# Kernel optimization log

Hardware: AMD Instinct MI355X
Metric: run time of the kernel (lower is better)

The kernel has to match this reference:

```python
import jax, jax.numpy as jnp
import numpy as np

STRIDES = (8, 16, 32)
NC = 80            # num_classes
BINS = 16          # dfl_bins
TOPK = 10          # tal_topk
TAL_ALPHA, TAL_BETA = 0.5, 6.0   # ultralytics TaskAlignedAssigner defaults
EPS = 1e-9
FOCAL_A, FOCAL_G = 0.25, 2.0
W_CLS, W_IOU, W_DFL = 0.5, 7.5, 1.5


def _make_grid(H, W, stride):
    ys, xs = jnp.meshgrid(jnp.arange(H, dtype=jnp.float32), jnp.arange(W, dtype=jnp.float32), indexing='ij')
    return jnp.stack([(xs + 0.5) * stride, (ys + 0.5) * stride], -1).reshape(H * W, 2)


def _flatten(p):
    # (B,C,H,W) -> cls (B,N,NC), dfl (B,N,4,BINS); channel layout = [4*BINS dfl | NC cls]
    B, C, H, W = p.shape
    p = p.transpose(0, 2, 3, 1).reshape(B, H * W, C)
    return p[..., 4 * BINS:], p[..., :4 * BINS].reshape(B, H * W, 4, BINS)


def _pairwise_iou(gt, pr):
    # gt (B,G,4), pr (B,N,4) -> iou (B,G,N)
    g = gt[:, :, None]
    p = pr[:, None]
    lt = jnp.maximum(g[..., :2], p[..., :2])
    rb = jnp.minimum(g[..., 2:], p[..., 2:])
    wh = jnp.clip(rb - lt, 0.0)
    inter = wh[..., 0] * wh[..., 1]
    ag = (g[..., 2] - g[..., 0]) * (g[..., 3] - g[..., 1])
    ap = jnp.clip(p[..., 2] - p[..., 0], 0.0) * jnp.clip(p[..., 3] - p[..., 1], 0.0)
    return inter / (ag + ap - inter + EPS)


def _ciou_loss(p, t):
    # elementwise CIoU loss, (...,4) xyxy -> (...)
    px1, py1, px2, py2 = p[..., 0], p[..., 1], p[..., 2], p[..., 3]
    tx1, ty1, tx2, ty2 = t[..., 0], t[..., 1], t[..., 2], t[..., 3]
    w1, h1 = px2 - px1, py2 - py1
    w2, h2 = tx2 - tx1, ty2 - ty1
    inter = jnp.clip(jnp.minimum(px2, tx2) - jnp.maximum(px1, tx1), 0.0) * \
            jnp.clip(jnp.minimum(py2, ty2) - jnp.maximum(py1, ty1), 0.0)
    union = w1 * h1 + w2 * h2 - inter + EPS
    iou = inter / union
    cw = jnp.maximum(px2, tx2) - jnp.minimum(px1, tx1)
    ch = jnp.maximum(py2, ty2) - jnp.minimum(py1, ty1)
    c2 = cw * cw + ch * ch + EPS
    rho2 = ((px1 + px2 - tx1 - tx2) ** 2 + (py1 + py2 - ty1 - ty2) ** 2) / 4.0
    v = (4.0 / np.pi ** 2) * (jnp.arctan(w2 / (h2 + EPS)) - jnp.arctan(w1 / (h1 + EPS))) ** 2
    alpha = jax.lax.stop_gradient(v / (v - iou + (1.0 + EPS)))
    return 1.0 - (iou - rho2 / c2 - v * alpha)


def _tal_assign(cls_prob, pred_boxes, grids, gt_bboxes, gt_labels):
    B, N, C = cls_prob.shape
    G = gt_bboxes.shape[1]
    idx = jnp.broadcast_to(gt_labels[:, None, :], (B, N, G))
    scores = jnp.take_along_axis(cls_prob, idx, axis=2).transpose(0, 2, 1)  # (B,G,N)
    overlaps = _pairwise_iou(gt_bboxes, pred_boxes)                          # (B,G,N)
    align = scores ** TAL_ALPHA * overlaps ** TAL_BETA
    x, y = grids[:, 0], grids[:, 1]
    in_gts = ((x[None, None] > gt_bboxes[..., 0:1]) & (x[None, None] < gt_bboxes[..., 2:3]) &
              (y[None, None] > gt_bboxes[..., 1:2]) & (y[None, None] < gt_bboxes[..., 3:4]))
    metric = jnp.where(in_gts, align, 0.0)
    vals, idxs = jax.lax.top_k(metric, TOPK)                                 # (B,G,TOPK)
    bi = jnp.arange(B)[:, None, None]
    gi = jnp.arange(G)[None, :, None]
    topk_mask = jnp.zeros((B, G, N), bool).at[bi, gi, idxs].set(vals > EPS)
    mask_pos = topk_mask & in_gts
    multi = mask_pos.sum(1) > 1                                              # (B,N)
    is_max = jnp.argmax(overlaps, 1)[:, None, :] == jnp.arange(G)[None, :, None]
    mask_pos = jnp.where(multi[:, None, :], is_max, mask_pos)
    fg = mask_pos.any(1)                                                     # (B,N)
    matched = jnp.argmax(mask_pos, 1)                                        # (B,N)
    mi = jnp.where(fg, matched, -1)
    b2 = jnp.arange(B)[:, None]
    tb = gt_bboxes[b2, matched]                                              # (B,N,4)
    tl = gt_labels[b2, matched]                                              # (B,N)
    mpf = mask_pos.astype(align.dtype)
    align_m = align * mpf
    ov_m = overlaps * mpf
    norm = (align_m * ov_m.max(-1, keepdims=True) / (align_m.max(-1, keepdims=True) + EPS)).max(1)
    ts = jax.nn.one_hot(tl, C, dtype=align.dtype) * norm[..., None] * fg[..., None]
    return ts, tb, fg, mi


def _dfl_targets(gt_bboxes, mi, fgf, grids, stride_map):
    # vectorized version of _make_dfl_targets: soft two-bin scatter per coord
    B, N = mi.shape
    b2 = jnp.arange(B)[:, None]
    boxes = gt_bboxes[b2, jnp.maximum(mi, 0)]                                # (B,N,4)
    cx, cy = grids[:, 0], grids[:, 1]
    d = jnp.stack([jnp.clip(cx - boxes[..., 0], 0.0), jnp.clip(cy - boxes[..., 1], 0.0),
                   jnp.clip(boxes[..., 2] - cx, 0.0), jnp.clip(boxes[..., 3] - cy, 0.0)], -1)
    d = jnp.clip(d / stride_map[None, :, None], 0.0, BINS - 1 - 1e-6)
    lo = jnp.floor(d)
    a = d - lo
    lo_i = lo.astype(jnp.int32)
    up_i = jnp.minimum(lo_i + 1, BINS - 1)
    td = jax.nn.one_hot(lo_i, BINS) * (1.0 - a)[..., None] + jax.nn.one_hot(up_i, BINS) * a[..., None]
    return td * fgf[..., None, None]                                         # (B,N,4,BINS)


def _focal_sum(logits, targets):
    logits = logits.reshape(-1, NC)
    targets = targets.reshape(-1, NC)
    p = jax.nn.sigmoid(logits)
    # stable BCE-with-logits
    ce = jnp.maximum(logits, 0.0) - logits * targets + jnp.log1p(jnp.exp(-jnp.abs(logits)))
    p_t = p * targets + (1.0 - p) * (1.0 - targets)
    a_t = targets * FOCAL_A + (1.0 - targets) * (1.0 - FOCAL_A)
    return (a_t * (1.0 - p_t) ** FOCAL_G * ce).sum()


def _loss(p0, p1, p2, gt_bboxes, gt_labels):
    cls_l, dfl_l, grid_l, str_l = [], [], [], []
    for p, s in zip((p0, p1, p2), STRIDES):
        c, d = _flatten(p)
        cls_l.append(c)
        dfl_l.append(d)
        H, W = p.shape[2], p.shape[3]
        grid_l.append(_make_grid(H, W, s))
        str_l.append(jnp.full((H * W,), float(s), jnp.float32))
    all_cls = jnp.concatenate(cls_l, 1)       # (B,N,NC)
    all_dfl = jnp.concatenate(dfl_l, 1)       # (B,N,4,BINS)
    grids = jnp.concatenate(grid_l, 0)        # (N,2)
    stride_map = jnp.concatenate(str_l, 0)    # (N,)
    # DFL decode: expectation over bins * stride -> ltrb -> xyxy
    dist = (jax.nn.softmax(all_dfl, -1) * jnp.arange(BINS, dtype=jnp.float32)).sum(-1) * stride_map[None, :, None]
    cx, cy = grids[:, 0], grids[:, 1]
    pred_boxes = jnp.stack([cx - dist[..., 0], cy - dist[..., 1], cx + dist[..., 2], cy + dist[..., 3]], -1)
    # assignment under stop_gradient (torch.no_grad in the original)
    cls_prob = jax.lax.stop_gradient(jax.nn.sigmoid(all_cls))
    pb_sg = jax.lax.stop_gradient(pred_boxes)
    ts, tb, fg, mi = _tal_assign(cls_prob, pb_sg, grids, gt_bboxes, gt_labels)
    ts = jax.lax.stop_gradient(ts)
    tb = jax.lax.stop_gradient(tb)
    fgf = fg.astype(jnp.float32)
    den = jnp.maximum(fg.sum(), 1).astype(jnp.float32)
    loss_iou = (_ciou_loss(pred_boxes, tb) * fgf).sum() / den
    tdfl = _dfl_targets(gt_bboxes, mi, fgf, grids, stride_map)
    loss_dfl = -(tdfl * jax.nn.log_softmax(all_dfl, -1)).sum() / den
    loss_cls = _focal_sum(all_cls, ts) / den
    return jnp.stack([W_IOU * loss_iou, W_DFL * loss_dfl, W_CLS * loss_cls])


def setup_inputs() -> dict:
    key = jax.random.key(0)
    ks = jax.random.split(key, 5)
    B, G = 16, 32
    p0 = jax.random.normal(ks[0], (B, 4 * BINS + NC, 80, 80), jnp.float32)
    p1 = jax.random.normal(ks[1], (B, 4 * BINS + NC, 40, 40), jnp.float32)
    p2 = jax.random.normal(ks[2], (B, 4 * BINS + NC, 20, 20), jnp.float32)
    u = jax.random.uniform(ks[3], (B, G, 4), jnp.float32)
    x1 = u[..., 0] * 560.0
    y1 = u[..., 1] * 560.0
    w = u[..., 2] * 140.0 + 20.0
    h = u[..., 3] * 140.0 + 20.0
    gt_bboxes = jnp.stack([x1, y1, jnp.minimum(x1 + w, 640.0), jnp.minimum(y1 + h, 640.0)], -1)
    gt_labels = jax.random.randint(ks[4], (B, G), 0, NC, jnp.int32)
    return {"p0": p0, "p1": p1, "p2": p2, "gt_bboxes": gt_bboxes, "gt_labels": gt_labels}


def reference(p0, p1, p2, gt_bboxes, gt_labels):
    return _loss(p0, p1, p2, gt_bboxes, gt_labels)
```

## Files before the change

kernel.cpp:

```cpp
#include <hip/hip_runtime.h>
#include <hip/hip_bf16.h>
#include <math.h>

#define NCC 80
#define BINS 16
#define NCH 144
#define NB 16
#define NG 32
#define NA 8400
#define HW0 6400
#define HW1 1600
#define HW2 400
#define TOPKK 10
#define EPSF 1e-9f
#define MAXC 832
#define MAXFG (NB*NG*TOPKK)
#define FGB (MAXFG/4)
#define NMASK (NB*NA)
#define DEC_BLOCKS 525
#define FOCAL_BLOCKS 2625
#define MAIN_BLOCKS (DEC_BLOCKS + FOCAL_BLOCKS)

__device__ __forceinline__ void anchor_geom(int n, float& cx, float& cy, float& st){
    if(n < HW0){ int y=n/80, x=n-y*80; st=8.f; cx=(x+0.5f)*8.f; cy=(y+0.5f)*8.f; }
    else if(n < HW0+HW1){ int m=n-HW0; int y=m/40, x=m-y*40; st=16.f; cx=(x+0.5f)*16.f; cy=(y+0.5f)*16.f; }
    else { int m=n-(HW0+HW1); int y=m/20, x=m-y*20; st=32.f; cx=(x+0.5f)*32.f; cy=(y+0.5f)*32.f; }
}

__device__ __forceinline__ const float* level_base(const float* p0, const float* p1, const float* p2,
                                                   int b, int n, int& m, int& hw){
    if(n < HW0){ m=n; hw=HW0; return p0 + (size_t)b*NCH*HW0; }
    if(n < HW0+HW1){ m=n-HW0; hw=HW1; return p1 + (size_t)b*NCH*HW1; }
    m=n-(HW0+HW1); hw=HW2; return p2 + (size_t)b*NCH*HW2;
}

__device__ __forceinline__ float iou_gp(float gx1,float gy1,float gx2,float gy2,
                                        float px1,float py1,float px2,float py2){
    float ltx = fmaxf(gx1, px1), lty = fmaxf(gy1, py1);
    float rbx = fminf(gx2, px2), rby = fminf(gy2, py2);
    float w = fmaxf(rbx-ltx, 0.f), h = fmaxf(rby-lty, 0.f);
    float inter = w*h;
    float ag = (gx2-gx1)*(gy2-gy1);
    float ap = fmaxf(px2-px1,0.f)*fmaxf(py2-py1,0.f);
    return inter/(ag+ap-inter+EPSF);
}

__device__ __forceinline__ float focal0(float x, float& p, float& ce0){
    float ax = fabsf(x);
    float e  = __expf(-ax);
    float r  = 1.f/(1.f+e);
    p   = (x >= 0.f) ? r : 1.f - r;
    ce0 = fmaxf(x,0.f) + __logf(1.f+e);
    return 0.75f*p*p*ce0;
}

__global__ __launch_bounds__(256) void k_main(const float* __restrict__ p0, const float* __restrict__ p1,
                                              const float* __restrict__ p2, float* __restrict__ boxc,
                                              unsigned* __restrict__ maskg, float* __restrict__ amax,
                                              float* __restrict__ omax, int* __restrict__ cnt,
                                              int* __restrict__ done, float* __restrict__ pcls){
    int tid = threadIdx.x;
    if(blockIdx.x < DEC_BLOCKS){
        int l = blockIdx.x*256 + tid;
        maskg[l] = 0u;
        if(l < NB*NG){ amax[l] = 0.f; omax[l] = 0.f; }
        if(l == 0){ *cnt = 0; *done = 0; }
        int q = l % 2100;
        int j = (l / 2100) & 3;
        int b = l / 8400;
        const float* pl; int hw, m, n0, D; float st;
        if(q < 1600){ pl=p0; hw=HW0; m=4*q;        n0=m;         D=80; st=8.f; }
        else if(q < 2000){ pl=p1; hw=HW1; m=4*(q-1600); n0=HW0+m;     D=40; st=16.f; }
        else { pl=p2; hw=HW2; m=4*(q-2000); n0=HW0+HW1+m; D=20; st=32.f; }
        const float* ch = pl + ((size_t)b*NCH + j*BINS)*hw + m;
        float4 v[BINS];
        float4 mx = make_float4(-1e30f,-1e30f,-1e30f,-1e30f);
        #pragma unroll
        for(int k=0;k<BINS;k++){
            v[k] = *(const float4*)(ch + (size_t)k*hw);
            mx.x=fmaxf(mx.x,v[k].x); mx.y=fmaxf(mx.y,v[k].y);
            mx.z=fmaxf(mx.z,v[k].z); mx.w=fmaxf(mx.w,v[k].w);
        }
        float4 s = make_float4(0,0,0,0), acc = make_float4(0,0,0,0);
        #pragma unroll
        for(int k=0;k<BINS;k++){
            float fk=(float)k; float e;
            e=__expf(v[k].x-mx.x); s.x+=e; acc.x+=e*fk;
            e=__expf(v[k].y-mx.y); s.y+=e; acc.y+=e*fk;
            e=__expf(v[k].z-mx.z); s.z+=e; acc.z+=e*fk;
            e=__expf(v[k].w-mx.w); s.w+=e; acc.w+=e*fk;
        }
        float4 d = make_float4(acc.x/s.x*st, acc.y/s.y*st, acc.z/s.z*st, acc.w/s.w*st);
        int row = m / D, col = m - row*D;
        float cy = (row+0.5f)*st;
        float cx0=(col+0.5f)*st, cx1=(col+1.5f)*st, cx2=(col+2.5f)*st, cx3=(col+3.5f)*st;
        float4 o;
        if(j==0)      o = make_float4(cx0-d.x, cx1-d.y, cx2-d.z, cx3-d.w);
        else if(j==1) o = make_float4(cy -d.x, cy -d.y, cy -d.z, cy -d.w);
        else if(j==2) o = make_float4(cx0+d.x, cx1+d.y, cx2+d.z, cx3+d.w);
        else          o = make_float4(cy +d.x, cy +d.y, cy +d.z, cy +d.w);
        *(float4*)(boxc + (size_t)j*NB*NA + (size_t)b*NA + n0) = o;
    } else {
        __shared__ float s4[4];
        int blk = blockIdx.x - DEC_BLOCKS;
        int t = blk*256 + tid;
        float acc = 0.f;
        #pragma unroll
        for(int it=0; it<4; ++it){
            int i4 = t + it*672000;
            const float4* src;
            if(i4 < 2048000){
                int b = i4 / 128000; int r = i4 - b*128000;
                src = (const float4*)(p0 + (size_t)b*921600 + 409600) + r;
            } else if(i4 < 2560000){
                int j = i4 - 2048000; int b = j / 32000; int r = j - b*32000;
                src = (const float4*)(p1 + (size_t)b*230400 + 102400) + r;
            } else {
                int j = i4 - 2560000; int b = j / 8000; int r = j - b*8000;
                src = (const float4*)(p2 + (size_t)b*57600 + 25600) + r;
            }
            float4 x4 = *src;
            float p, c;
            acc += focal0(x4.x, p, c);
            acc += focal0(x4.y, p, c);
            acc += focal0(x4.z, p, c);
            acc += focal0(x4.w, p, c);
        }
        #pragma unroll
        for(int off=32; off; off>>=1) acc += __shfl_down(acc, off);
        if((tid&63)==0) s4[tid>>6] = acc;
        __syncthreads();
        if(tid==0) pcls[blk] = s4[0]+s4[1]+s4[2]+s4[3];
    }
}

__global__ __launch_bounds__(256) void k_assign(const float* __restrict__ p0, const float* __restrict__ p1,
                                                const float* __restrict__ p2, const float* __restrict__ boxc,
                                                const float* __restrict__ gtb, const int* __restrict__ gtl,
                                                unsigned* __restrict__ maskg){
    __shared__ float metric[MAXC];
    __shared__ int   candn[MAXC];
    __shared__ float rv[4]; __shared__ int ri[4];
    __shared__ float sbest;
    int g = blockIdx.x, b = blockIdx.y, tid = threadIdx.x;
    const float* gb = gtb + ((size_t)b*NG + g)*4;
    float gx1=gb[0], gy1=gb[1], gx2=gb[2], gy2=gb[3];
    int label = gtl[b*NG+g];
    const float* bx1 = boxc + (size_t)b*NA;
    const float* by1 = bx1 + (size_t)NB*NA;
    const float* bx2 = by1 + (size_t)NB*NA;
    const float* by2 = bx2 + (size_t)NB*NA;

    int xs[3], ys[3], nxv[3], cc[3];
    #pragma unroll
    for(int lvl=0; lvl<3; lvl++){
        float s = (float)(8<<lvl); int D = 80>>lvl;
        int x0 = max(0, (int)floorf(gx1/s - 0.5f));
        int x1 = min(D-1, (int)ceilf (gx2/s - 0.5f));
        int y0 = max(0, (int)floorf(gy1/s - 0.5f));
        int y1 = min(D-1, (int)ceilf (gy2/s - 0.5f));
        xs[lvl]=x0; ys[lvl]=y0;
        nxv[lvl]=max(0, x1-x0+1);
        int nyv=max(0, y1-y0+1);
        cc[lvl]=nxv[lvl]*nyv;
    }
    int t0 = cc[0], t01 = cc[0]+cc[1], total = t01+cc[2];

    for(int c=tid; c<total; c+=256){
        int lvl, rel;
        if(c < t0){ lvl=0; rel=c; }
        else if(c < t01){ lvl=1; rel=c-t0; }
        else { lvl=2; rel=c-t01; }
        int yy = ys[lvl] + rel / nxv[lvl];
        int xx = xs[lvl] + rel % nxv[lvl];
        int D = 80>>lvl; float s = (float)(8<<lvl);
        int off = (lvl==0)?0:((lvl==1)?HW0:(HW0+HW1));
        int n = off + yy*D + xx;
        float cx = (xx+0.5f)*s, cy = (yy+0.5f)*s;
        float met = 0.f;
        if((cx>gx1)&&(cx<gx2)&&(cy>gy1)&&(cy<gy2)){
            float ov = iou_gp(gx1,gy1,gx2,gy2, bx1[n],by1[n],bx2[n],by2[n]);
            int m,hw; const float* base = level_base(p0,p1,p2,b,n,m,hw);
            float x = base[(size_t)(4*BINS+label)*hw + m];
            float sg = 1.f/(1.f+__expf(-x));
            float o2 = ov*ov;
            met = sqrtf(sg)*(o2*o2*o2);
        }
        metric[c] = met; candn[c] = n;
    }
    __syncthreads();

    for(int k=0;k<TOPKK;k++){
        float bv = -1.f; int bi = 0x7fffffff;
        for(int c=tid; c<total; c+=256){
            float v = metric[c];
            if(v > bv){ bv=v; bi=c; }
        }
        #pragma unroll
        for(int o=1; o<64; o<<=1){
            float ov = __shfl_xor(bv, o);
            int   oi = __shfl_xor(bi, o);
            if(ov > bv || (ov == bv && oi < bi)){ bv=ov; bi=oi; }
        }
        if((tid&63)==0){ rv[tid>>6]=bv; ri[tid>>6]=bi; }
        __syncthreads();
        if(tid==0){
            float fb=rv[0]; int fi=ri[0];
            #pragma unroll
            for(int w=1; w<4; w++)
                if(rv[w]>fb || (rv[w]==fb && ri[w]<fi)){ fb=rv[w]; fi=ri[w]; }
            sbest = fb;
            if(fb > EPSF){
                metric[fi] = -1.f;
                atomicOr(&maskg[(size_t)b*NA + candn[fi]], 1u<<g);
            }
        }
        __syncthreads();
        if(sbest <= EPSF) break;
    }
}

__global__ __launch_bounds__(256) void k_resolve(const float* __restrict__ p0, const float* __restrict__ p1,
                                                 const float* __restrict__ p2, const float* __restrict__ boxc,
                                                 const float* __restrict__ gtb, const int* __restrict__ gtl,
                                                 const unsigned* __restrict__ maskg,
                                                 float* __restrict__ amax, float* __restrict__ omax,
                                                 int* __restrict__ cnt, unsigned* __restrict__ fglist,
                                                 float* __restrict__ fgalign, float* __restrict__ fgx){
    __shared__ float sgt[NG*4];
    __shared__ int wcnt[4];
    __shared__ int sbase;
    int tid = threadIdx.x; int b = blockIdx.y;
    int wv = tid >> 6, lane = tid & 63;
    if(tid < NG*4) sgt[tid] = gtb[(size_t)b*NG*4 + tid];
    __syncthreads();
    int n = blockIdx.x*256 + tid;
    size_t bn = (size_t)b*NA + n;
    unsigned mask = (n < NA) ? maskg[bn] : 0u;
    bool fg = (mask != 0u);

    int match = 0; float ov = 0.f, av = 0.f, x = 0.f;
    if(fg){
        float px1 = boxc[bn], py1 = boxc[(size_t)NB*NA+bn],
              px2 = boxc[2*(size_t)NB*NA+bn], py2 = boxc[3*(size_t)NB*NA+bn];
        if(__popc(mask) > 1){
            float best = -1.f; int bi = 0;
            for(int g=0; g<NG; g++){
                float o = iou_gp(sgt[g*4],sgt[g*4+1],sgt[g*4+2],sgt[g*4+3],px1,py1,px2,py2);
                if(o > best){ best=o; bi=g; }
            }
            match = bi; ov = best;
        } else {
            match = __ffs(mask)-1;
            ov = iou_gp(sgt[match*4],sgt[match*4+1],sgt[match*4+2],sgt[match*4+3],px1,py1,px2,py2);
        }
        int label = gtl[b*NG+match];
        int m,hw; const float* base = level_base(p0,p1,p2,b,n,m,hw);
        x = base[(size_t)(4*BINS+label)*hw + m];
        float sg = 1.f/(1.f+__expf(-x));
        float ov2 = ov*ov;
        av = sqrtf(sg)*(ov2*ov2*ov2);
        atomicMax((int*)&amax[b*NG+match], __float_as_int(av));
        atomicMax((int*)&omax[b*NG+match], __float_as_int(ov));
    }
    unsigned long long bal = __ballot(fg);
    if(lane==0) wcnt[wv] = __popcll(bal);
    __syncthreads();
    if(tid==0){
        int tot = wcnt[0]+wcnt[1]+wcnt[2]+wcnt[3];
        sbase = tot ? atomicAdd(cnt, tot) : 0;
    }
    __syncthreads();
    if(fg){
        int woff = 0;
        for(int w=0; w<wv; w++) woff += wcnt[w];
        int before = __popcll(bal & ((1ull<<lane)-1ull));
        int pos = sbase + woff + before;
        fglist[pos]  = (unsigned)bn | ((unsigned)match << 18);
        fgalign[pos] = av;
        fgx[pos]     = x;
    }
}

__global__ __launch_bounds__(256) void k_fgfin(const float* __restrict__ p0, const float* __restrict__ p1,
                                               const float* __restrict__ p2, const float* __restrict__ boxc,
                                               const float* __restrict__ gtb,
                                               const float* __restrict__ amax, const float* __restrict__ omax,
                                               const int* __restrict__ cnt, const unsigned* __restrict__ fglist,
                                               const float* __restrict__ fgalign, const float* __restrict__ fgx,
                                               float* __restrict__ piou, float* __restrict__ pdfl,
                                               float* __restrict__ pfix, const float* __restrict__ pcls,
                                               int* __restrict__ done, float* __restrict__ out){
    __shared__ float s4[12];
    __shared__ float sa[4], sb[4], sc[4], sd[4];
    __shared__ int slast;
    int tid = threadIdx.x, wv = tid>>6, lane = tid&63;
    int i = blockIdx.x*4 + wv;
    float iou_l = 0.f, dfl_l = 0.f, fix_l = 0.f;
    if(i < *cnt){
        unsigned e = fglist[i];
        int bn = e & 0x3FFFF;
        int g  = e >> 18;
        int b  = bn / NA;
        int n  = bn - b*NA;
        float align = fgalign[i];
        float norm = align * omax[b*NG+g] / (amax[b*NG+g] + EPSF);
        const float* gb = gtb + ((size_t)b*NG+g)*4;
        float tx1=gb[0], ty1=gb[1], tx2=gb[2], ty2=gb[3];
        float px1 = boxc[bn], py1 = boxc[(size_t)NB*NA+bn],
              px2 = boxc[2*(size_t)NB*NA+bn], py2 = boxc[3*(size_t)NB*NA+bn];
        int m,hw; const float* base = level_base(p0,p1,p2,b,n,m,hw);
        float cx,cy,st; anchor_geom(n,cx,cy,st);
        int j = lane>>4, k = lane&15;
        float x = base[(size_t)lane*hw + m];
        float dt = (j==0)?(cx-tx1):((j==1)?(cy-ty1):((j==2)?(tx2-cx):(ty2-cy)));
        float d = fminf(fmaxf(dt,0.f)/st, 14.999999f);
        float lo = floorf(d); float a = d-lo;
        int li = (int)lo; int ui = min(li+1, BINS-1);
        float mx = x;
        #pragma unroll
        for(int o=1;o<16;o<<=1) mx = fmaxf(mx, __shfl_xor(mx,o));
        float ex = __expf(x-mx);
        float se = ex;
        #pragma unroll
        for(int o=1;o<16;o<<=1) se += __shfl_xor(se,o);
        float lse = mx + __logf(se);
        float coef = ((k==li)?(1.f-a):0.f) + ((k==ui)?a:0.f);
        dfl_l = -coef*(x-lse);
        if(lane==0){
            float w1=px2-px1, h1=py2-py1, w2=tx2-tx1, h2=ty2-ty1;
            float inter = fmaxf(fminf(px2,tx2)-fmaxf(px1,tx1),0.f) *
                          fmaxf(fminf(py2,ty2)-fmaxf(py1,ty1),0.f);
            float uni = w1*h1 + w2*h2 - inter + EPSF;
            float iou = inter/uni;
            float cwd = fmaxf(px2,tx2)-fminf(px1,tx1);
            float chd = fmaxf(py2,ty2)-fminf(py1,ty1);
            float c2 = cwd*cwd + chd*chd + EPSF;
            float dx = px1+px2-tx1-tx2, dy = py1+py2-ty1-ty2;
            float rho2 = (dx*dx + dy*dy)*0.25f;
            float dv = atanf(w2/(h2+EPSF)) - atanf(w1/(h1+EPSF));
            float v = 0.40528473456935108577f*dv*dv;
            float alpha = v/(v - iou + 1.f + EPSF);
            iou_l = 1.f - (iou - rho2/c2 - v*alpha);
            float fx = fgx[i];
            float p, ce0;
            float f0 = focal0(fx, p, ce0);
            float tv = norm;
            float cet = ce0 - fx*tv;
            float pt = p*tv + (1.f-p)*(1.f-tv);
            float at = 0.25f*tv + 0.75f*(1.f-tv);
            float om = 1.f-pt;
            fix_l = at*om*om*cet - f0;
        }
    }
    #pragma unroll
    for(int o=32; o; o>>=1){
        iou_l += __shfl_down(iou_l, o);
        dfl_l += __shfl_down(dfl_l, o);
        fix_l += __shfl_down(fix_l, o);
    }
    if(lane==0){ s4[wv]=iou_l; s4[4+wv]=dfl_l; s4[8+wv]=fix_l; }
    __syncthreads();
    if(tid==0){
        piou[blockIdx.x] = s4[0]+s4[1]+s4[2]+s4[3];
        pdfl[blockIdx.x] = s4[4]+s4[5]+s4[6]+s4[7];
        pfix[blockIdx.x] = s4[8]+s4[9]+s4[10]+s4[11];
        __threadfence();
        int old = atomicAdd(done, 1);
        slast = (old == FGB-1) ? 1 : 0;
    }
    __syncthreads();
    if(!slast) return;
    __threadfence();
    float A = 0.f, B = 0.f, C = 0.f, D = 0.f;
    for(int t=tid; t<FOCAL_BLOCKS; t+=256) A += pcls[t];
    for(int t=tid; t<FGB; t+=256){ B += piou[t]; C += pdfl[t]; D += pfix[t]; }
    #pragma unroll
    for(int o=32; o; o>>=1){
        A += __shfl_down(A, o);
        B += __shfl_down(B, o);
        C += __shfl_down(C, o);
        D += __shfl_down(D, o);
    }
    if(lane==0){ sa[wv]=A; sb[wv]=B; sc[wv]=C; sd[wv]=D; }
    __syncthreads();
    if(tid==0){
        float a = sa[0]+sa[1]+sa[2]+sa[3];
        float bb = sb[0]+sb[1]+sb[2]+sb[3];
        float cc2 = sc[0]+sc[1]+sc[2]+sc[3];
        float dd = sd[0]+sd[1]+sd[2]+sd[3];
        int c = *cnt;
        float den = (float)(c > 1 ? c : 1);
        out[0] = 7.5f * bb / den;
        out[1] = 1.5f * cc2 / den;
        out[2] = 0.5f * (a + dd) / den;
    }
}

extern "C" void kernel_launch(void* const* d_in, const int* in_sizes, int n_in,
                              void* d_out, int out_size, void* d_ws, size_t ws_size,
                              hipStream_t stream) {
    (void)in_sizes; (void)n_in; (void)out_size; (void)ws_size;
    const float* p0  = (const float*)d_in[0];
    const float* p1  = (const float*)d_in[1];
    const float* p2  = (const float*)d_in[2];
    const float* gtb = (const float*)d_in[3];
    const int*   gtl = (const int*)d_in[4];
    float* out = (float*)d_out;

    char* ws = (char*)d_ws;
    const size_t COMP = (size_t)NB*NA*4;
    size_t off = 0;
    int*      cnt    = (int*)     (ws + off); off += 16;
    int*      done   = (int*)     (ws + off); off += 16;
    float*    amax   = (float*)   (ws + off); off += NB*NG*4;
    float*    omax   = (float*)   (ws + off); off += NB*NG*4;
    unsigned* maskg  = (unsigned*)(ws + off); off += COMP;
    float*    boxc   = (float*)   (ws + off); off += 4*COMP;
    unsigned* fglist = (unsigned*)(ws + off); off += MAXFG*4;
    float*    fgalign= (float*)   (ws + off); off += MAXFG*4;
    float*    fgx    = (float*)   (ws + off); off += MAXFG*4;
    float*    pcls   = (float*)   (ws + off); off += FOCAL_BLOCKS*4;
    float*    piou   = (float*)   (ws + off); off += FGB*4;
    float*    pdfl   = (float*)   (ws + off); off += FGB*4;
    float*    pfix   = (float*)   (ws + off); off += FGB*4;

    dim3 blk(256);
    k_main   <<<MAIN_BLOCKS,   blk, 0, stream>>>(p0,p1,p2, boxc, maskg, amax, omax, cnt, done, pcls);
    k_assign <<<dim3(NG,NB),   blk, 0, stream>>>(p0,p1,p2, boxc, gtb, gtl, maskg);
    k_resolve<<<dim3(33,NB),   blk, 0, stream>>>(p0,p1,p2, boxc, gtb, gtl, maskg,
                                                 amax, omax, cnt, fglist, fgalign, fgx);
    k_fgfin  <<<FGB,           blk, 0, stream>>>(p0,p1,p2, boxc, gtb, amax, omax,
                                                 cnt, fglist, fgalign, fgx, piou, pdfl, pfix,
                                                 pcls, done, out);
}
```

Before: 171.5 us.

## Precompute DFL log-sum-exp in decode and process one foreground per thread

The decode stage now stores the per-side log-sum-exp of the DFL logits in a new workspace array. The foreground kernel can then compute the DFL loss from just two gathered bins per side instead of a full 64-lane wavefront reduction. Each thread handles one foreground entry over 20 blocks, where before each wavefront handled one entry over 1280 blocks. The last-block atomic reduction is replaced by a separate single-block final kernel. This costs an extra 4×NB×NA float write in the decode stage and one more kernel launch, and FGB2=20 covers only 5120 foreground slots.

```diff
diff --git a/kernel.cpp b/kernel.cpp
--- a/kernel.cpp
+++ b/kernel.cpp
@@ -15,7 +15,7 @@
 #define EPSF 1e-9f
 #define MAXC 832
 #define MAXFG (NB*NG*TOPKK)
-#define FGB (MAXFG/4)
+#define FGB2 20
 #define NMASK (NB*NA)
 #define DEC_BLOCKS 525
 #define FOCAL_BLOCKS 2625
@@ -56,15 +56,16 @@
 
 __global__ __launch_bounds__(256) void k_main(const float* __restrict__ p0, const float* __restrict__ p1,
                                               const float* __restrict__ p2, float* __restrict__ boxc,
+                                              float* __restrict__ lsev,
                                               unsigned* __restrict__ maskg, float* __restrict__ amax,
                                               float* __restrict__ omax, int* __restrict__ cnt,
-                                              int* __restrict__ done, float* __restrict__ pcls){
+                                              float* __restrict__ pcls){
     int tid = threadIdx.x;
     if(blockIdx.x < DEC_BLOCKS){
         int l = blockIdx.x*256 + tid;
         maskg[l] = 0u;
         if(l < NB*NG){ amax[l] = 0.f; omax[l] = 0.f; }
-        if(l == 0){ *cnt = 0; *done = 0; }
+        if(l == 0) *cnt = 0;
         int q = l % 2100;
         int j = (l / 2100) & 3;
         int b = l / 8400;
@@ -90,6 +91,9 @@
             e=__expf(v[k].z-mx.z); s.z+=e; acc.z+=e*fk;
             e=__expf(v[k].w-mx.w); s.w+=e; acc.w+=e*fk;
         }
+        float4 lse = make_float4(mx.x+__logf(s.x), mx.y+__logf(s.y),
+                                 mx.z+__logf(s.z), mx.w+__logf(s.w));
+        *(float4*)(lsev + (size_t)j*NB*NA + (size_t)b*NA + n0) = lse;
         float4 d = make_float4(acc.x/s.x*st, acc.y/s.y*st, acc.z/s.z*st, acc.w/s.w*st);
         int row = m / D, col = m - row*D;
         float cy = (row+0.5f)*st;
@@ -282,20 +286,17 @@
     }
 }
 
-__global__ __launch_bounds__(256) void k_fgfin(const float* __restrict__ p0, const float* __restrict__ p1,
-                                               const float* __restrict__ p2, const float* __restrict__ boxc,
-                                               const float* __restrict__ gtb,
-                                               const float* __restrict__ amax, const float* __restrict__ omax,
-                                               const int* __restrict__ cnt, const unsigned* __restrict__ fglist,
-                                               const float* __restrict__ fgalign, const float* __restrict__ fgx,
-                                               float* __restrict__ piou, float* __restrict__ pdfl,
-                                               float* __restrict__ pfix, const float* __restrict__ pcls,
-                                               int* __restrict__ done, float* __restrict__ out){
-    __shared__ float s4[12];
-    __shared__ float sa[4], sb[4], sc[4], sd[4];
-    __shared__ int slast;
+__global__ __launch_bounds__(256) void k_fg(const float* __restrict__ p0, const float* __restrict__ p1,
+                                            const float* __restrict__ p2, const float* __restrict__ boxc,
+                                            const float* __restrict__ lsev, const float* __restrict__ gtb,
+                                            const float* __restrict__ amax, const float* __restrict__ omax,
+                                            const int* __restrict__ cnt, const unsigned* __restrict__ fglist,
+                                            const float* __restrict__ fgalign, const float* __restrict__ fgx,
+                                            float* __restrict__ piou, float* __restrict__ pdfl,
+                                            float* __restrict__ pfix){
+    __shared__ float siou[4], sdfl[4], sfix[4];
     int tid = threadIdx.x, wv = tid>>6, lane = tid&63;
-    int i = blockIdx.x*4 + wv;
+    int i = blockIdx.x*256 + tid;
     float iou_l = 0.f, dfl_l = 0.f, fix_l = 0.f;
     if(i < *cnt){
         unsigned e = fglist[i];
@@ -311,47 +312,40 @@
               px2 = boxc[2*(size_t)NB*NA+bn], py2 = boxc[3*(size_t)NB*NA+bn];
         int m,hw; const float* base = level_base(p0,p1,p2,b,n,m,hw);
         float cx,cy,st; anchor_geom(n,cx,cy,st);
-        int j = lane>>4, k = lane&15;
-        float x = base[(size_t)lane*hw + m];
-        float dt = (j==0)?(cx-tx1):((j==1)?(cy-ty1):((j==2)?(tx2-cx):(ty2-cy)));
-        float d = fminf(fmaxf(dt,0.f)/st, 14.999999f);
-        float lo = floorf(d); float a = d-lo;
-        int li = (int)lo; int ui = min(li+1, BINS-1);
-        float mx = x;
-        #pragma unroll
-        for(int o=1;o<16;o<<=1) mx = fmaxf(mx, __shfl_xor(mx,o));
-        float ex = __expf(x-mx);
-        float se = ex;
-        #pragma unroll
-        for(int o=1;o<16;o<<=1) se += __shfl_xor(se,o);
-        float lse = mx + __logf(se);
-        float coef = ((k==li)?(1.f-a):0.f) + ((k==ui)?a:0.f);
-        dfl_l = -coef*(x-lse);
-        if(lane==0){
-            float w1=px2-px1, h1=py2-py1, w2=tx2-tx1, h2=ty2-ty1;
-            float inter = fmaxf(fminf(px2,tx2)-fmaxf(px1,tx1),0.f) *
-                          fmaxf(fminf(py2,ty2)-fmaxf(py1,ty1),0.f);
-            float uni = w1*h1 + w2*h2 - inter + EPSF;
-            float iou = inter/uni;
-            float cwd = fmaxf(px2,tx2)-fminf(px1,tx1);
-            float chd = fmaxf(py2,ty2)-fminf(py1,ty1);
-            float c2 = cwd*cwd + chd*chd + EPSF;
-            float dx = px1+px2-tx1-tx2, dy = py1+py2-ty1-ty2;
-            float rho2 = (dx*dx + dy*dy)*0.25f;
-            float dv = atanf(w2/(h2+EPSF)) - atanf(w1/(h1+EPSF));
-            float v = 0.40528473456935108577f*dv*dv;
-            float alpha = v/(v - iou + 1.f + EPSF);
-            iou_l = 1.f - (iou - rho2/c2 - v*alpha);
-            float fx = fgx[i];
-            float p, ce0;
-            float f0 = focal0(fx, p, ce0);
-            float tv = norm;
-            float cet = ce0 - fx*tv;
-            float pt = p*tv + (1.f-p)*(1.f-tv);
-            float at = 0.25f*tv + 0.75f*(1.f-tv);
-            float om = 1.f-pt;
-            fix_l = at*om*om*cet - f0;
-        }
+        float dt4[4] = { cx-tx1, cy-ty1, tx2-cx, ty2-cy };
+        #pragma unroll
+        for(int j=0;j<4;j++){
+            float d = fminf(fmaxf(dt4[j],0.f)/st, 14.999999f);
+            float lo = floorf(d); float a = d-lo;
+            int li = (int)lo; int ui = min(li+1, BINS-1);
+            float lse = lsev[(size_t)j*NB*NA + bn];
+            float xlo = base[(size_t)(j*BINS+li)*hw + m];
+            float xup = base[(size_t)(j*BINS+ui)*hw + m];
+            dfl_l += -((1.f-a)*(xlo-lse) + a*(xup-lse));
+        }
+        float w1=px2-px1, h1=py2-py1, w2=tx2-tx1, h2=ty2-ty1;
+        float inter = fmaxf(fminf(px2,tx2)-fmaxf(px1,tx1),0.f) *
+                      fmaxf(fminf(py2,ty2)-fmaxf(py1,ty1),0.f);
+        float uni = w1*h1 + w2*h2 - inter + EPSF;
+        float iou = inter/uni;
+        float cwd = fmaxf(px2,tx2)-fminf(px1,tx1);
+        float chd = fmaxf(py2,ty2)-fminf(py1,ty1);
+        float c2 = cwd*cwd + chd*chd + EPSF;
+        float dx = px1+px2-tx1-tx2, dy = py1+py2-ty1-ty2;
+        float rho2 = (dx*dx + dy*dy)*0.25f;
+        float dv = atanf(w2/(h2+EPSF)) - atanf(w1/(h1+EPSF));
+        float v = 0.40528473456935108577f*dv*dv;
+        float alpha = v/(v - iou + 1.f + EPSF);
+        iou_l = 1.f - (iou - rho2/c2 - v*alpha);
+        float fx = fgx[i];
+        float p, ce0;
+        float f0 = focal0(fx, p, ce0);
+        float tv = norm;
+        float cet = ce0 - fx*tv;
+        float pt = p*tv + (1.f-p)*(1.f-tv);
+        float at = 0.25f*tv + 0.75f*(1.f-tv);
+        float om = 1.f-pt;
+        fix_l = at*om*om*cet - f0;
     }
     #pragma unroll
     for(int o=32; o; o>>=1){
@@ -359,22 +353,23 @@
         dfl_l += __shfl_down(dfl_l, o);
         fix_l += __shfl_down(fix_l, o);
     }
-    if(lane==0){ s4[wv]=iou_l; s4[4+wv]=dfl_l; s4[8+wv]=fix_l; }
+    if(lane==0){ siou[wv]=iou_l; sdfl[wv]=dfl_l; sfix[wv]=fix_l; }
     __syncthreads();
     if(tid==0){
-        piou[blockIdx.x] = s4[0]+s4[1]+s4[2]+s4[3];
-        pdfl[blockIdx.x] = s4[4]+s4[5]+s4[6]+s4[7];
-        pfix[blockIdx.x] = s4[8]+s4[9]+s4[10]+s4[11];
-        __threadfence();
-        int old = atomicAdd(done, 1);
-        slast = (old == FGB-1) ? 1 : 0;
-    }
-    __syncthreads();
-    if(!slast) return;
-    __threadfence();
+        piou[blockIdx.x] = siou[0]+siou[1]+siou[2]+siou[3];
+        pdfl[blockIdx.x] = sdfl[0]+sdfl[1]+sdfl[2]+sdfl[3];
+        pfix[blockIdx.x] = sfix[0]+sfix[1]+sfix[2]+sfix[3];
+    }
+}
+
+__global__ __launch_bounds__(256) void k_final(const float* __restrict__ pcls, const float* __restrict__ piou,
+                                               const float* __restrict__ pdfl, const float* __restrict__ pfix,
+                                               const int* __restrict__ cnt, float* __restrict__ out){
+    __shared__ float sa[4], sb[4], sc[4], sd[4];
+    int tid = threadIdx.x, wv = tid>>6, lane = tid&63;
     float A = 0.f, B = 0.f, C = 0.f, D = 0.f;
     for(int t=tid; t<FOCAL_BLOCKS; t+=256) A += pcls[t];
-    for(int t=tid; t<FGB; t+=256){ B += piou[t]; C += pdfl[t]; D += pfix[t]; }
+    if(tid < FGB2){ B = piou[tid]; C = pdfl[tid]; D = pfix[tid]; }
     #pragma unroll
     for(int o=32; o; o>>=1){
         A += __shfl_down(A, o);
@@ -385,14 +380,14 @@
     if(lane==0){ sa[wv]=A; sb[wv]=B; sc[wv]=C; sd[wv]=D; }
     __syncthreads();
     if(tid==0){
-        float a = sa[0]+sa[1]+sa[2]+sa[3];
+        float a  = sa[0]+sa[1]+sa[2]+sa[3];
         float bb = sb[0]+sb[1]+sb[2]+sb[3];
-        float cc2 = sc[0]+sc[1]+sc[2]+sc[3];
+        float cc = sc[0]+sc[1]+sc[2]+sc[3];
         float dd = sd[0]+sd[1]+sd[2]+sd[3];
         int c = *cnt;
         float den = (float)(c > 1 ? c : 1);
         out[0] = 7.5f * bb / den;
-        out[1] = 1.5f * cc2 / den;
+        out[1] = 1.5f * cc / den;
         out[2] = 0.5f * (a + dd) / den;
     }
 }
@@ -412,25 +407,25 @@
     const size_t COMP = (size_t)NB*NA*4;
     size_t off = 0;
     int*      cnt    = (int*)     (ws + off); off += 16;
-    int*      done   = (int*)     (ws + off); off += 16;
     float*    amax   = (float*)   (ws + off); off += NB*NG*4;
     float*    omax   = (float*)   (ws + off); off += NB*NG*4;
     unsigned* maskg  = (unsigned*)(ws + off); off += COMP;
     float*    boxc   = (float*)   (ws + off); off += 4*COMP;
+    float*    lsev   = (float*)   (ws + off); off += 4*COMP;
     unsigned* fglist = (unsigned*)(ws + off); off += MAXFG*4;
     float*    fgalign= (float*)   (ws + off); off += MAXFG*4;
     float*    fgx    = (float*)   (ws + off); off += MAXFG*4;
     float*    pcls   = (float*)   (ws + off); off += FOCAL_BLOCKS*4;
-    float*    piou   = (float*)   (ws + off); off += FGB*4;
-    float*    pdfl   = (float*)   (ws + off); off += FGB*4;
-    float*    pfix   = (float*)   (ws + off); off += FGB*4;
+    float*    piou   = (float*)   (ws + off); off += FGB2*4;
+    float*    pdfl   = (float*)   (ws + off); off += FGB2*4;
+    float*    pfix   = (float*)   (ws + off); off += FGB2*4;
 
     dim3 blk(256);
-    k_main   <<<MAIN_BLOCKS,   blk, 0, stream>>>(p0,p1,p2, boxc, maskg, amax, omax, cnt, done, pcls);
+    k_main   <<<MAIN_BLOCKS,   blk, 0, stream>>>(p0,p1,p2, boxc, lsev, maskg, amax, omax, cnt, pcls);
     k_assign <<<dim3(NG,NB),   blk, 0, stream>>>(p0,p1,p2, boxc, gtb, gtl, maskg);
     k_resolve<<<dim3(33,NB),   blk, 0, stream>>>(p0,p1,p2, boxc, gtb, gtl, maskg,
                                                  amax, omax, cnt, fglist, fgalign, fgx);
-    k_fgfin  <<<FGB,           blk, 0, stream>>>(p0,p1,p2, boxc, gtb, amax, omax,
-                                                 cnt, fglist, fgalign, fgx, piou, pdfl, pfix,
-                                                 pcls, done, out);
-}
+    k_fg     <<<FGB2,          blk, 0, stream>>>(p0,p1,p2, boxc, lsev, gtb, amax, omax,
+                                                 cnt, fglist, fgalign, fgx, piou, pdfl, pfix);
+    k_final  <<<1,             blk, 0, stream>>>(pcls, piou, pdfl, pfix, cnt, out);
+}
```

After: 144.6 us (median of 2 runs). 15.7% less time.
